# Optimization experiments

Measured on AMD Instinct MI355X. Metric: run time of the kernel, lower is better.

## Reference

```python
import jax, jax.numpy as jnp
import numpy as np

T, D, F, E, K = 8192, 1024, 4096, 8, 2


def setup_inputs() -> dict:
    key = jax.random.key(0)
    ks = jax.random.split(key, 8)
    s = 0.02
    return {
        "gate_inputs": jax.random.normal(ks[0], (T, D), jnp.float32),
        "inputs": jax.random.normal(ks[1], (T, D), jnp.float32),
        "Wg": jax.random.normal(ks[2], (D, E), jnp.float32) * s,
        "bg": jnp.zeros((E,), jnp.float32),
        "w1": jax.random.normal(ks[3], (E, D, F), jnp.float32) * s,
        "b1": jnp.zeros((E, F), jnp.float32),
        "w2": jax.random.normal(ks[4], (E, F, D), jnp.float32) * s,
        "b2": jnp.zeros((E, D), jnp.float32),
    }


def reference(gate_inputs, inputs, Wg, bg, w1, b1, w2, b2):
    # gate + top-k routing (torch.topk returns sorted descending, as lax.top_k)
    logits = gate_inputs @ Wg + bg                      # [T, E]
    weights, selected = jax.lax.top_k(logits, K)        # [T, K]
    weights = jax.nn.softmax(weights.astype(jnp.float32), axis=1).astype(inputs.dtype)
    # scatter top-k weights into dense combine matrix [T, E]
    t_idx = jnp.arange(inputs.shape[0])[:, None]
    combine = jnp.zeros(logits.shape, inputs.dtype).at[t_idx, selected].add(weights)

    # loop over experts via scan (E is a small structural dim), accumulate weighted outputs
    def body(acc, params):
        W1, B1, W2, B2, ce = params                     # ce: [T] combine weight for this expert
        h = jax.nn.gelu(inputs @ W1 + B1)               # [T, F]
        y = h @ W2 + B2                                 # [T, D]
        return acc + ce[:, None] * y, None

    out, _ = jax.lax.scan(body, jnp.zeros_like(inputs), (w1, b1, w2, b2, combine.T))
    return out
```

## Files before the change

### kernel.cpp

```cpp
#include <hip/hip_runtime.h>
#include <stdint.h>

#define T_TOK 8192
#define DMODEL 1024
#define FDIM 4096
#define NEXP 8
#define NROWS 16384
#define MAXT 80

#define GATE_BLKS 2048
#define CVT_BLKS  4096
#define TRW_BLKS  16384
#define PREP_BLKS (GATE_BLKS + CVT_BLKS + TRW_BLKS)

typedef __bf16 bf16x8 __attribute__((ext_vector_type(8)));
typedef float f32x4 __attribute__((ext_vector_type(4)));
#define AS1 __attribute__((address_space(1)))
#define AS3 __attribute__((address_space(3)))

__device__ __forceinline__ unsigned short f2bf(float f) {
  union { float f; unsigned u; } v; v.f = f;
  unsigned r = v.u + 0x7fffu + ((v.u >> 16) & 1u);
  return (unsigned short)(r >> 16);
}
__device__ __forceinline__ float bflo(unsigned u) {
  union { unsigned u; float f; } v; v.u = u << 16; return v.f;
}
__device__ __forceinline__ float bfhi(unsigned u) {
  union { unsigned u; float f; } v; v.u = u & 0xffff0000u; return v.f;
}

__device__ __forceinline__ void tile_tr_gld(
    const float* __restrict__ in, unsigned short* __restrict__ out,
    int Kdim, int Ndim, int e, int kt, int ng, float* lds)
{
  size_t ebase = (size_t)e * Kdim * Ndim;
  const int tid = threadIdx.x, lane = tid & 63, wave = tid >> 6;
  const int k0 = kt * 64, n0 = ng * 64;
  const int lr = lane >> 4, lc = (lane & 15) * 4;
#pragma unroll
  for (int it = 0; it < 4; ++it) {
    int c = wave * 4 + it;
    const float* src = in + ebase + (size_t)(k0 + c * 4 + lr) * Ndim + n0 + lc;
    __builtin_amdgcn_global_load_lds(
        (const AS1 void*)src, (AS3 void*)((char*)lds + c * 1024), 16, 0, 0);
  }
  asm volatile("s_waitcnt vmcnt(0)" ::: "memory");
  __syncthreads();
  int n = tid >> 2, k16 = (tid & 3) * 16;
  union { unsigned short h[16]; uint4 q[2]; } pk;
#pragma unroll
  for (int j = 0; j < 16; ++j)
    pk.h[j] = f2bf(lds[(k16 + j) * 64 + n]);
  unsigned short* dst = out + ebase + ((size_t)kt * Ndim + n0 + n) * 64 + k16;
  *(uint4*)dst = pk.q[0];
  *(uint4*)(dst + 8) = pk.q[1];
}

__global__ __launch_bounds__(256) void prep_kernel(
    const float* __restrict__ gx, const float* __restrict__ Wg,
    const float* __restrict__ bg, int* __restrict__ sel,
    float* __restrict__ wts, int* __restrict__ counts,
    const float* __restrict__ inputs, unsigned short* __restrict__ Xb,
    const float* __restrict__ w1, unsigned short* __restrict__ W1T,
    const float* __restrict__ w2, unsigned short* __restrict__ W2T)
{
  __shared__ __align__(16) float tr_lds[64 * 64];
  int b = blockIdx.x;
  if (b < GATE_BLKS) {
    int t = b * 4 + (threadIdx.x >> 6);
    int lane = threadIdx.x & 63;
    const float* row = gx + (size_t)t * DMODEL;
    float acc[NEXP];
#pragma unroll
    for (int e = 0; e < NEXP; ++e) acc[e] = 0.f;
    for (int d = lane; d < DMODEL; d += 64) {
      float x = row[d];
      const float* wgr = Wg + (size_t)d * NEXP;
#pragma unroll
      for (int e = 0; e < NEXP; ++e) acc[e] += x * wgr[e];
    }
#pragma unroll
    for (int off = 32; off > 0; off >>= 1) {
#pragma unroll
      for (int e = 0; e < NEXP; ++e) acc[e] += __shfl_down(acc[e], off);
    }
    if (lane == 0) {
      float lg[NEXP];
#pragma unroll
      for (int e = 0; e < NEXP; ++e) lg[e] = acc[e] + bg[e];
      int i1 = 0; float v1 = lg[0];
#pragma unroll
      for (int e = 1; e < NEXP; ++e) if (lg[e] > v1) { v1 = lg[e]; i1 = e; }
      int i2 = -1; float v2 = -3.4e38f;
#pragma unroll
      for (int e = 0; e < NEXP; ++e) if (e != i1 && lg[e] > v2) { v2 = lg[e]; i2 = e; }
      float ez = __expf(v2 - v1);
      float s = 1.f / (1.f + ez);
      sel[t*2] = i1; sel[t*2+1] = i2;
      wts[t*2] = s;  wts[t*2+1] = ez * s;
      atomicAdd(&counts[i1], 1);
      atomicAdd(&counts[i2], 1);
    }
  } else if (b < GATE_BLKS + CVT_BLKS) {
    int i = (b - GATE_BLKS) * 256 + threadIdx.x;
    const float4* in4 = (const float4*)inputs;
    float4 v0 = in4[(size_t)i*2], v1 = in4[(size_t)i*2 + 1];
    union { unsigned short u[8]; uint4 q; } r;
    r.u[0]=f2bf(v0.x); r.u[1]=f2bf(v0.y); r.u[2]=f2bf(v0.z); r.u[3]=f2bf(v0.w);
    r.u[4]=f2bf(v1.x); r.u[5]=f2bf(v1.y); r.u[6]=f2bf(v1.z); r.u[7]=f2bf(v1.w);
    ((uint4*)Xb)[i] = r.q;
  } else {
    int bp = b - (GATE_BLKS + CVT_BLKS);
    if (bp < 8192) {
      int e = bp >> 10, tile = bp & 1023;
      tile_tr_gld(w1, W1T, DMODEL, FDIM, e, tile >> 6, tile & 63, tr_lds);
    } else {
      bp -= 8192;
      int e = bp >> 10, tile = bp & 1023;
      tile_tr_gld(w2, W2T, FDIM, DMODEL, e, tile >> 4, tile & 15, tr_lds);
    }
  }
}

__global__ __launch_bounds__(256) void scan_build_kernel(
    const int* __restrict__ counts, int* __restrict__ offsets,
    int* __restrict__ ntiles, int* __restrict__ t_e, int* __restrict__ t_r,
    int* __restrict__ t_rend)
{
  __shared__ int sc[8], soff[9], stile[9];
  int tid = threadIdx.x;
  if (tid < 8) sc[tid] = counts[tid];
  __syncthreads();
  if (tid == 0) {
    int off = 0, tl = 0;
#pragma unroll
    for (int e = 0; e < NEXP; ++e) {
      soff[e] = off; stile[e] = tl;
      off += sc[e];
      tl += (sc[e] + 255) >> 8;
    }
    soff[8] = off; stile[8] = tl;
  }
  __syncthreads();
  int ntot = stile[8];
  for (int idx = tid; idx < ntot; idx += 256) {
    int e = 0;
#pragma unroll
    for (int q = 0; q < NEXP; ++q) if (idx >= stile[q + 1]) e = q + 1;
    int r = (idx - stile[e]) * 256;
    t_e[idx] = e; t_r[idx] = soff[e] + r; t_rend[idx] = soff[e] + sc[e];
  }
  if (tid < 9) offsets[tid] = soff[tid];
  if (tid == 0) *ntiles = ntot;
}

__global__ __launch_bounds__(256) void scatter_kernel(
    const int* __restrict__ sel, int* __restrict__ cursors,
    const int* __restrict__ offsets, int* __restrict__ token_list,
    int* __restrict__ slot_list)
{
  int t = blockIdx.x * 256 + threadIdx.x;
  int lane = threadIdx.x & 63;
  unsigned long long ltmask = (lane == 63) ? 0x7fffffffffffffffull
                                           : ((1ull << lane) - 1ull);
#pragma unroll
  for (int k = 0; k < 2; ++k) {
    int e = sel[t*2 + k];
#pragma unroll
    for (int ex = 0; ex < NEXP; ++ex) {
      unsigned long long m = __ballot(e == ex);
      if (m == 0ull) continue;
      if (e == ex) {
        int leader = __ffsll((unsigned long long)m) - 1;
        int cnt = __popcll(m);
        int base = 0;
        if (lane == leader) base = atomicAdd(&cursors[ex], cnt);
        base = __shfl(base, leader);
        int r = offsets[ex] + base + __popcll(m & ltmask);
        token_list[r] = t;
        slot_list[r] = t*2 + k;
      }
    }
  }
}

template<bool G1>
__global__ __launch_bounds__(512, 2) void gemm256_kernel(
    const unsigned short* __restrict__ A, const unsigned short* __restrict__ B,
    const float* __restrict__ b1, const int* __restrict__ token_list,
    const int* __restrict__ slot_list,
    const int* __restrict__ tile_e, const int* __restrict__ tile_r,
    const int* __restrict__ tile_rend, const int* __restrict__ ntiles,
    unsigned short* __restrict__ outp)
{
  constexpr int KDIM = G1 ? DMODEL : FDIM;
  constexpr int NKT  = KDIM / 64;
  constexpr int NOUT = G1 ? FDIM : DMODEL;
  constexpr int KTB  = NOUT * 64;

  int bid = blockIdx.x;
  int nb, bt;
  if constexpr (G1) {
    int xcd = bid & 7, idx = bid >> 3;
    nb = xcd * 2 + (idx & 1);
    bt = idx >> 1;
  } else {
    nb = bid & 3;
    bt = bid >> 2;
  }
  if (bt >= *ntiles) return;
  const int e = tile_e[bt], row0 = tile_r[bt], rend = tile_rend[bt];
  const int n0 = nb * 256;

  const int tid = threadIdx.x, lane = tid & 63, wave = tid >> 6;
  extern __shared__ __align__(16) char smem[];

  const int lr8 = lane >> 3, g8 = lane & 7, ch = g8 ^ lr8;

  int mA[2], mB[2];
#pragma unroll
  for (int p = 0; p < 2; ++p)
    mA[p] = (wave < 4) ? (p*64 + wave*16) : (128 + p*64 + (wave-4)*16);
#pragma unroll
  for (int nh = 0; nh < 2; ++nh)
    mB[nh] = (wave >> 1)*64 + nh*32 + (wave & 1)*16;

  const unsigned short* eB = B + (size_t)e * KDIM * NOUT;
  unsigned aoffs[2][2], boffs[2][2];
#pragma unroll
  for (int p = 0; p < 2; ++p)
#pragma unroll
    for (int l = 0; l < 2; ++l) {
      int m = mA[p] + l*8 + lr8;
      int row = row0 + m; if (row > NROWS - 1) row = NROWS - 1;
      int arow = G1 ? token_list[row] : row;
      aoffs[p][l] = (unsigned)arow * KDIM + ch*8;
      int mb = mB[p] + l*8 + lr8;
      boffs[p][l] = (unsigned)((n0 + mb) * 64 + ch*8);
    }

  auto stage_half = [&](int p, int ktn, int bsel) {
    char* base = smem + bsel * 65536;
    if (p < 2) {
      const int kb = ktn * 64;
#pragma unroll
      for (int l = 0; l < 2; ++l)
        __builtin_amdgcn_global_load_lds(
            (const AS1 void*)(A + aoffs[p][l] + kb),
            (AS3 void*)(base + ((mA[p] + l*8) << 7)), 16, 0, 0);
    } else {
      const int nh = p - 2;
      const unsigned short* bk = eB + (size_t)ktn * KTB;
#pragma unroll
      for (int l = 0; l < 2; ++l)
        __builtin_amdgcn_global_load_lds(
            (const AS1 void*)(bk + boffs[nh][l]),
            (AS3 void*)(base + 32768 + ((mB[nh] + l*8) << 7)), 16, 0, 0);
    }
  };

  f32x4 acc[8][4] = {};
  bf16x8 aR[4][2];
  bf16x8 bR[2][2][2];
  const int wr = wave >> 2, wc = wave & 3;
  const int lm = lane & 15, lk = lane >> 4, l7 = lane & 7;
  const unsigned abase = (unsigned)(wr*128 + lm) * 128;
  const unsigned bbase = 32768u + (unsigned)(wc*64 + lm) * 128;
  const unsigned kx0 = (unsigned)((lk ^ l7) << 4);
  const unsigned kx1 = (unsigned)(((4 + lk) ^ l7) << 4);

  auto rdA = [&](const char* base, int mh) {
#pragma unroll
    for (int i = 0; i < 4; ++i) {
      const char* pA = base + abase + mh*8192 + i*2048;
      aR[i][0] = *(const bf16x8*)(pA + kx0);
      aR[i][1] = *(const bf16x8*)(pA + kx1);
    }
  };
  auto rdB = [&](const char* base, int nh) {
#pragma unroll
    for (int jj = 0; jj < 2; ++jj) {
      const char* pB = base + bbase + nh*4096 + jj*2048;
      bR[nh][jj][0] = *(const bf16x8*)(pB + kx0);
      bR[nh][jj][1] = *(const bf16x8*)(pB + kx1);
    }
  };
  auto mm = [&](int mh, int nh) {
    __builtin_amdgcn_s_setprio(1);
#pragma unroll
    for (int i = 0; i < 4; ++i)
#pragma unroll
      for (int jj = 0; jj < 2; ++jj) {
        acc[mh*4+i][nh*2+jj] = __builtin_amdgcn_mfma_f32_16x16x32_bf16(
            aR[i][0], bR[nh][jj][0], acc[mh*4+i][nh*2+jj], 0, 0, 0);
        acc[mh*4+i][nh*2+jj] = __builtin_amdgcn_mfma_f32_16x16x32_bf16(
            aR[i][1], bR[nh][jj][1], acc[mh*4+i][nh*2+jj], 0, 0, 0);
      }
    __builtin_amdgcn_s_setprio(0);
  };

  stage_half(0, 0, 0);
  stage_half(2, 0, 0);
  stage_half(3, 0, 0);
  stage_half(1, 0, 0);

  for (int kt = 0; kt < NKT; ++kt) {
    const int b = kt & 1;
    const int nxt = b ^ 1;
    const char* base = smem + b * 65536;
    const bool pre = (kt + 1 < NKT);
    if (pre) {
      stage_half(0, kt + 1, nxt);
      asm volatile("s_waitcnt vmcnt(6)" ::: "memory");
    } else {
      asm volatile("s_waitcnt vmcnt(4)" ::: "memory");
    }
    __builtin_amdgcn_s_barrier();
    __builtin_amdgcn_sched_barrier(0);
    rdA(base, 0); rdB(base, 0);
    asm volatile("s_waitcnt lgkmcnt(0)" ::: "memory");
    __builtin_amdgcn_sched_barrier(0);
    mm(0, 0);
    __builtin_amdgcn_s_barrier();
    if (pre) {
      stage_half(2, kt + 1, nxt);
      asm volatile("s_waitcnt vmcnt(6)" ::: "memory");
    } else {
      asm volatile("s_waitcnt vmcnt(2)" ::: "memory");
    }
    __builtin_amdgcn_s_barrier();
    __builtin_amdgcn_sched_barrier(0);
    rdB(base, 1);
    asm volatile("s_waitcnt lgkmcnt(0)" ::: "memory");
    __builtin_amdgcn_sched_barrier(0);
    mm(0, 1);
    __builtin_amdgcn_s_barrier();
    if (pre) {
      stage_half(3, kt + 1, nxt);
      asm volatile("s_waitcnt vmcnt(6)" ::: "memory");
    } else {
      asm volatile("s_waitcnt vmcnt(0)" ::: "memory");
    }
    __builtin_amdgcn_s_barrier();
    __builtin_amdgcn_sched_barrier(0);
    rdA(base, 1);
    asm volatile("s_waitcnt lgkmcnt(0)" ::: "memory");
    __builtin_amdgcn_sched_barrier(0);
    mm(1, 1);
    __builtin_amdgcn_s_barrier();
    if (pre) stage_half(1, kt + 1, nxt);
    mm(1, 0);
    __builtin_amdgcn_s_barrier();
    __builtin_amdgcn_sched_barrier(0);
  }

  asm volatile("" ::: "memory");
  float bias[4] = {};
  if constexpr (G1) {
#pragma unroll
    for (int j = 0; j < 4; ++j) bias[j] = b1[(size_t)e * FDIM + n0 + wc*64 + j*16 + lm];
  }

  float* eps = (float*)smem;
#pragma unroll
  for (int c = 0; c < 8; ++c) {
    __syncthreads();
    if (wr == (c >> 2)) {
#pragma unroll
      for (int ii = 0; ii < 2; ++ii) {
        const int mi = (c & 3) * 2 + ii;
#pragma unroll
        for (int j = 0; j < 4; ++j) {
#pragma unroll
          for (int r = 0; r < 4; ++r) {
            float v = acc[mi][j][r];
            if constexpr (G1) {
              v += bias[j];
              float z2 = 1.5957691216f * (v + 0.044715f * v * v * v);
              v = v / (1.f + __expf(-z2));
            }
            eps[(ii*16 + lk*4 + r) * 260 + wc*64 + j*16 + lm] = v;
          }
        }
      }
    }
    __syncthreads();
#pragma unroll
    for (int u = 0; u < 2; ++u) {
      int item = u * 512 + tid;
      int lrow = item >> 5, c8 = (item & 31) * 8;
      int gr = row0 + c * 32 + lrow;
      if (gr < rend) {
        float4 v0 = *(const float4*)&eps[lrow * 260 + c8];
        float4 v1 = *(const float4*)&eps[lrow * 260 + c8 + 4];
        union { unsigned short u[8]; uint4 q; } pk;
        pk.u[0]=f2bf(v0.x); pk.u[1]=f2bf(v0.y); pk.u[2]=f2bf(v0.z); pk.u[3]=f2bf(v0.w);
        pk.u[4]=f2bf(v1.x); pk.u[5]=f2bf(v1.y); pk.u[6]=f2bf(v1.z); pk.u[7]=f2bf(v1.w);
        size_t orow;
        if constexpr (G1) orow = (size_t)gr * FDIM;
        else              orow = (size_t)slot_list[gr] * DMODEL;
        *(uint4*)(outp + orow + n0 + c8) = pk.q;
      }
    }
  }
}

__global__ __launch_bounds__(256) void combine_kernel(
    const unsigned short* __restrict__ ys, const float* __restrict__ wts,
    const int* __restrict__ sel, const float* __restrict__ b2,
    float* __restrict__ out)
{
  int i = blockIdx.x * 256 + threadIdx.x;
  int t = i >> 7, d8 = i & 127;
  float w0 = wts[t*2], w1 = wts[t*2 + 1];
  int e0 = sel[t*2], e1 = sel[t*2 + 1];
  const uint4* ys4 = (const uint4*)ys;
  uint4 ya = ys4[(size_t)(t*2) * 128 + d8];
  uint4 yb = ys4[(size_t)(t*2 + 1) * 128 + d8];
  const float4* b24 = (const float4*)b2;
  float4 c0a = b24[e0*256 + d8*2], c0b = b24[e0*256 + d8*2 + 1];
  float4 c1a = b24[e1*256 + d8*2], c1b = b24[e1*256 + d8*2 + 1];
  float4 o0, o1;
  o0.x = w0*(bflo(ya.x)+c0a.x) + w1*(bflo(yb.x)+c1a.x);
  o0.y = w0*(bfhi(ya.x)+c0a.y) + w1*(bfhi(yb.x)+c1a.y);
  o0.z = w0*(bflo(ya.y)+c0a.z) + w1*(bflo(yb.y)+c1a.z);
  o0.w = w0*(bfhi(ya.y)+c0a.w) + w1*(bfhi(yb.y)+c1a.w);
  o1.x = w0*(bflo(ya.z)+c0b.x) + w1*(bflo(yb.z)+c1b.x);
  o1.y = w0*(bfhi(ya.z)+c0b.y) + w1*(bfhi(yb.z)+c1b.y);
  o1.z = w0*(bflo(ya.w)+c0b.z) + w1*(bflo(yb.w)+c1b.z);
  o1.w = w0*(bfhi(ya.w)+c0b.w) + w1*(bfhi(yb.w)+c1b.w);
  float4* out4 = (float4*)out;
  out4[(size_t)t * 256 + d8*2]     = o0;
  out4[(size_t)t * 256 + d8*2 + 1] = o1;
}

extern "C" void kernel_launch(void* const* d_in, const int* in_sizes, int n_in,
                              void* d_out, int out_size, void* d_ws, size_t ws_size,
                              hipStream_t stream)
{
  const float* gate_inputs = (const float*)d_in[0];
  const float* inputs      = (const float*)d_in[1];
  const float* Wg          = (const float*)d_in[2];
  const float* bg          = (const float*)d_in[3];
  const float* w1          = (const float*)d_in[4];
  const float* b1          = (const float*)d_in[5];
  const float* w2          = (const float*)d_in[6];
  const float* b2          = (const float*)d_in[7];
  float* out = (float*)d_out;

  char* ws = (char*)d_ws;
  size_t o = 0;
  auto carve = [&](size_t bytes) { void* p = ws + o; o += (bytes + 255) & ~(size_t)255; return p; };
  unsigned short* Xb  = (unsigned short*)carve((size_t)T_TOK * DMODEL * 2);
  unsigned short* W1T = (unsigned short*)carve((size_t)NEXP * FDIM * DMODEL * 2);
  unsigned short* W2T = (unsigned short*)carve((size_t)NEXP * DMODEL * FDIM * 2);
  unsigned short* H   = (unsigned short*)carve((size_t)NROWS * FDIM * 2);
  unsigned short* ys  = (unsigned short*)carve((size_t)NROWS * DMODEL * 2);
  int*   sel          = (int*)carve((size_t)NROWS * 4);
  float* wts          = (float*)carve((size_t)NROWS * 4);
  int*   token_list   = (int*)carve((size_t)(NROWS + 256) * 4);
  int*   slot_list    = (int*)carve((size_t)(NROWS + 256) * 4);
  int*   ctrl         = (int*)carve(4096);
  int* counts  = ctrl;
  int* cursors = ctrl + 8;
  int* offsets = ctrl + 16;
  int* ntiles  = ctrl + 28;
  int* t_e     = ctrl + 32;
  int* t_r     = ctrl + 32 + MAXT;
  int* t_rend  = ctrl + 32 + 2 * MAXT;

  hipMemsetAsync(counts, 0, 64, stream);

  prep_kernel<<<PREP_BLKS, 256, 0, stream>>>(
      gate_inputs, Wg, bg, sel, wts, counts,
      inputs, Xb, w1, W1T, w2, W2T);
  scan_build_kernel<<<1, 256, 0, stream>>>(counts, offsets, ntiles, t_e, t_r, t_rend);
  scatter_kernel<<<T_TOK / 256, 256, 0, stream>>>(sel, cursors, offsets, token_list, slot_list);

  hipFuncSetAttribute((const void*)gemm256_kernel<true>,
                      hipFuncAttributeMaxDynamicSharedMemorySize, 131072);
  hipFuncSetAttribute((const void*)gemm256_kernel<false>,
                      hipFuncAttributeMaxDynamicSharedMemorySize, 131072);
  gemm256_kernel<true><<<8 * 2 * MAXT, 512, 131072, stream>>>(
      Xb, W1T, b1, token_list, nullptr, t_e, t_r, t_rend, ntiles, H);
  gemm256_kernel<false><<<4 * MAXT, 512, 131072, stream>>>(
      H, W2T, nullptr, nullptr, slot_list, t_e, t_r, t_rend, ntiles, ys);
  combine_kernel<<<(T_TOK * DMODEL / 8) / 256, 256, 0, stream>>>(ys, wts, sel, b2, out);
}
```

Before: 707.4 us.

## Double-buffer weight transpose tiles and count experts in scan kernel

The weight transpose now has each block handle 8 consecutive 64x64 tiles. It double-buffers the global-to-LDS loads so the next tile's fetch overlaps conversion of the current one, which cuts the transpose block count eightfold. Per-expert counting moves out of the gate path's global atomics and into the single-block scan kernel, which rereads sel and reduces the counts in LDS. This trades fewer global atomics and fewer block launches for a serial 16K-element pass in one block, plus doubled LDS per prep block that may lower occupancy.

```diff
diff --git a/kernel.cpp b/kernel.cpp
--- a/kernel.cpp
+++ b/kernel.cpp
@@ -10,8 +10,8 @@
 
 #define GATE_BLKS 2048
 #define CVT_BLKS  4096
-#define TRW_BLKS  16384
-#define PREP_BLKS (GATE_BLKS + CVT_BLKS + TRW_BLKS)
+#define TRP_BLKS  2048
+#define PREP_BLKS (GATE_BLKS + CVT_BLKS + TRP_BLKS)
 
 typedef __bf16 bf16x8 __attribute__((ext_vector_type(8)));
 typedef float f32x4 __attribute__((ext_vector_type(4)));
@@ -30,42 +30,56 @@
   union { unsigned u; float f; } v; v.u = u & 0xffff0000u; return v.f;
 }
 
-__device__ __forceinline__ void tile_tr_gld(
+__device__ __forceinline__ void tile_tr_pipe(
     const float* __restrict__ in, unsigned short* __restrict__ out,
-    int Kdim, int Ndim, int e, int kt, int ng, float* lds)
+    int Kdim, int Ndim, int e, int kt, int ng0, float* lds)
 {
   size_t ebase = (size_t)e * Kdim * Ndim;
   const int tid = threadIdx.x, lane = tid & 63, wave = tid >> 6;
-  const int k0 = kt * 64, n0 = ng * 64;
   const int lr = lane >> 4, lc = (lane & 15) * 4;
-#pragma unroll
-  for (int it = 0; it < 4; ++it) {
-    int c = wave * 4 + it;
-    const float* src = in + ebase + (size_t)(k0 + c * 4 + lr) * Ndim + n0 + lc;
-    __builtin_amdgcn_global_load_lds(
-        (const AS1 void*)src, (AS3 void*)((char*)lds + c * 1024), 16, 0, 0);
-  }
-  asm volatile("s_waitcnt vmcnt(0)" ::: "memory");
-  __syncthreads();
-  int n = tid >> 2, k16 = (tid & 3) * 16;
-  union { unsigned short h[16]; uint4 q[2]; } pk;
-#pragma unroll
-  for (int j = 0; j < 16; ++j)
-    pk.h[j] = f2bf(lds[(k16 + j) * 64 + n]);
-  unsigned short* dst = out + ebase + ((size_t)kt * Ndim + n0 + n) * 64 + k16;
-  *(uint4*)dst = pk.q[0];
-  *(uint4*)(dst + 8) = pk.q[1];
+  auto stage = [&](int i, int b) {
+    const int n0 = (ng0 + i) * 64;
+#pragma unroll
+    for (int it = 0; it < 4; ++it) {
+      int c = wave * 4 + it;
+      const float* src = in + ebase + (size_t)(kt * 64 + c * 4 + lr) * Ndim + n0 + lc;
+      __builtin_amdgcn_global_load_lds(
+          (const AS1 void*)src,
+          (AS3 void*)((char*)lds + b * 16384 + c * 1024), 16, 0, 0);
+    }
+  };
+  stage(0, 0);
+  for (int i = 0; i < 8; ++i) {
+    const int b = i & 1;
+    if (i + 1 < 8) {
+      stage(i + 1, b ^ 1);
+      asm volatile("s_waitcnt vmcnt(4)" ::: "memory");
+    } else {
+      asm volatile("s_waitcnt vmcnt(0)" ::: "memory");
+    }
+    __syncthreads();
+    const float* L = lds + b * 4096;
+    int n = tid >> 2, k16 = (tid & 3) * 16;
+    union { unsigned short h[16]; uint4 q[2]; } pk;
+#pragma unroll
+    for (int j = 0; j < 16; ++j)
+      pk.h[j] = f2bf(L[(k16 + j) * 64 + n]);
+    unsigned short* dst = out + ebase + ((size_t)kt * Ndim + (ng0 + i) * 64 + n) * 64 + k16;
+    *(uint4*)dst = pk.q[0];
+    *(uint4*)(dst + 8) = pk.q[1];
+    __syncthreads();
+  }
 }
 
 __global__ __launch_bounds__(256) void prep_kernel(
     const float* __restrict__ gx, const float* __restrict__ Wg,
     const float* __restrict__ bg, int* __restrict__ sel,
-    float* __restrict__ wts, int* __restrict__ counts,
+    float* __restrict__ wts,
     const float* __restrict__ inputs, unsigned short* __restrict__ Xb,
     const float* __restrict__ w1, unsigned short* __restrict__ W1T,
     const float* __restrict__ w2, unsigned short* __restrict__ W2T)
 {
-  __shared__ __align__(16) float tr_lds[64 * 64];
+  __shared__ __align__(16) float tr_lds[2 * 64 * 64];
   int b = blockIdx.x;
   if (b < GATE_BLKS) {
     int t = b * 4 + (threadIdx.x >> 6);
@@ -99,8 +113,6 @@
       float s = 1.f / (1.f + ez);
       sel[t*2] = i1; sel[t*2+1] = i2;
       wts[t*2] = s;  wts[t*2+1] = ez * s;
-      atomicAdd(&counts[i1], 1);
-      atomicAdd(&counts[i2], 1);
     }
   } else if (b < GATE_BLKS + CVT_BLKS) {
     int i = (b - GATE_BLKS) * 256 + threadIdx.x;
@@ -112,25 +124,36 @@
     ((uint4*)Xb)[i] = r.q;
   } else {
     int bp = b - (GATE_BLKS + CVT_BLKS);
-    if (bp < 8192) {
-      int e = bp >> 10, tile = bp & 1023;
-      tile_tr_gld(w1, W1T, DMODEL, FDIM, e, tile >> 6, tile & 63, tr_lds);
+    if (bp < 1024) {
+      int e = bp >> 7, rem = bp & 127;
+      tile_tr_pipe(w1, W1T, DMODEL, FDIM, e, rem >> 3, (rem & 7) * 8, tr_lds);
     } else {
-      bp -= 8192;
-      int e = bp >> 10, tile = bp & 1023;
-      tile_tr_gld(w2, W2T, FDIM, DMODEL, e, tile >> 4, tile & 15, tr_lds);
+      bp -= 1024;
+      int e = bp >> 7, rem = bp & 127;
+      tile_tr_pipe(w2, W2T, FDIM, DMODEL, e, rem >> 1, (rem & 1) * 8, tr_lds);
     }
   }
 }
 
 __global__ __launch_bounds__(256) void scan_build_kernel(
-    const int* __restrict__ counts, int* __restrict__ offsets,
+    const int* __restrict__ sel, int* __restrict__ offsets,
     int* __restrict__ ntiles, int* __restrict__ t_e, int* __restrict__ t_r,
     int* __restrict__ t_rend)
 {
   __shared__ int sc[8], soff[9], stile[9];
   int tid = threadIdx.x;
-  if (tid < 8) sc[tid] = counts[tid];
+  if (tid < 8) sc[tid] = 0;
+  __syncthreads();
+  int cnt[NEXP];
+#pragma unroll
+  for (int e = 0; e < NEXP; ++e) cnt[e] = 0;
+  for (int i = tid; i < NROWS; i += 256) {
+    int v = sel[i];
+#pragma unroll
+    for (int e = 0; e < NEXP; ++e) cnt[e] += (v == e) ? 1 : 0;
+  }
+#pragma unroll
+  for (int e = 0; e < NEXP; ++e) if (cnt[e]) atomicAdd(&sc[e], cnt[e]);
   __syncthreads();
   if (tid == 0) {
     int off = 0, tl = 0;
@@ -462,7 +485,6 @@
   int*   token_list   = (int*)carve((size_t)(NROWS + 256) * 4);
   int*   slot_list    = (int*)carve((size_t)(NROWS + 256) * 4);
   int*   ctrl         = (int*)carve(4096);
-  int* counts  = ctrl;
   int* cursors = ctrl + 8;
   int* offsets = ctrl + 16;
   int* ntiles  = ctrl + 28;
@@ -470,12 +492,12 @@
   int* t_r     = ctrl + 32 + MAXT;
   int* t_rend  = ctrl + 32 + 2 * MAXT;
 
-  hipMemsetAsync(counts, 0, 64, stream);
+  hipMemsetAsync(ctrl, 0, 64, stream);
 
   prep_kernel<<<PREP_BLKS, 256, 0, stream>>>(
-      gate_inputs, Wg, bg, sel, wts, counts,
+      gate_inputs, Wg, bg, sel, wts,
       inputs, Xb, w1, W1T, w2, W2T);
-  scan_build_kernel<<<1, 256, 0, stream>>>(counts, offsets, ntiles, t_e, t_r, t_rend);
+  scan_build_kernel<<<1, 256, 0, stream>>>(sel, offsets, ntiles, t_e, t_r, t_rend);
   scatter_kernel<<<T_TOK / 256, 256, 0, stream>>>(sel, cursors, offsets, token_list, slot_list);
 
   hipFuncSetAttribute((const void*)gemm256_kernel<true>,
```

New measurement: 590.5 us. -16.5%, faster.
